# Kernel tuning notes

Measured on AMD Instinct MI355X. Metric: run time of the kernel, lower is better.

The kernel has to match this reference:

```python
import jax, jax.numpy as jnp
import numpy as np

DIM = 1024
HEADS = 16
DIM_HEAD = 64
INNER = HEADS * DIM_HEAD  # 1024
SCALE = DIM_HEAD ** -0.5


def setup_inputs() -> dict:
    key = jax.random.key(0)
    k_x, k_qkv, k_ow, k_ob = jax.random.split(key, 4)
    B, N = 4, 2048
    x = jax.random.normal(k_x, (B, N, DIM), dtype=jnp.float32)
    # nn.Linear weights stored as [out, in] in torch; keep [in, out] for x @ W.
    w_qkv = jax.random.normal(k_qkv, (DIM, 3 * INNER), dtype=jnp.float32) * (DIM ** -0.5)
    w_out = jax.random.normal(k_ow, (INNER, DIM), dtype=jnp.float32) * (INNER ** -0.5)
    b_out = jax.random.normal(k_ob, (DIM,), dtype=jnp.float32) * 0.01
    return {"x": x, "w_qkv": w_qkv, "w_out": w_out, "b_out": b_out}


def reference(x, w_qkv, w_out, b_out):
    B, N, _ = x.shape
    qkv = x @ w_qkv  # [B, N, 3*inner]
    q, k, v = jnp.split(qkv, 3, axis=-1)
    # [B, N, inner] -> [B, H, N, dh]
    def to_heads(t):
        return t.reshape(B, N, HEADS, DIM_HEAD).transpose(0, 2, 1, 3)
    q, k, v = to_heads(q), to_heads(k), to_heads(v)
    attn = jnp.einsum("bhqd,bhkd->bhqk", q, k) * SCALE  # [B, H, N, N]
    attn = jax.nn.softmax(attn, axis=-1)
    out = jnp.einsum("bhqk,bhkd->bhqd", attn, v)  # [B, H, N, dh]
    out = out.transpose(0, 2, 1, 3).reshape(B, N, INNER)
    return out @ w_out + b_out
```

## Files before the change

### kernel.cpp

```cpp
#include <hip/hip_runtime.h>
#include <hip/hip_bf16.h>
#include <stdint.h>

typedef __attribute__((ext_vector_type(4))) float f32x4;
typedef __attribute__((ext_vector_type(8))) short s16x8;
typedef __attribute__((ext_vector_type(4))) short s16x4;

#define DEV static __device__ __forceinline__

constexpr int B_ = 4, H_ = 16, N_ = 2048;
constexpr float CL_ = 0.18033688011112042f;

DEV short f2bf(float x) {
  __hip_bfloat16 h = __float2bfloat16(x);
  return *reinterpret_cast<short*>(&h);
}

DEV uint32_t cvtpk(float lo, float hi) {
  uint32_t r;
  asm("v_cvt_pk_bf16_f32 %0, %1, %2" : "=v"(r) : "v"(lo), "v"(hi));
  return r;
}

DEV void gload16(const void* g, void* l) {
  __builtin_amdgcn_global_load_lds((const __attribute__((address_space(1))) void*)g,
                                   (__attribute__((address_space(3))) void*)l, 16, 0, 0);
}

__global__ void k_cvt(const float* __restrict__ x, short* __restrict__ xb) {
  int i = (blockIdx.x * 256 + threadIdx.x) * 8;
  const float4* p = reinterpret_cast<const float4*>(x + i);
  float4 a = p[0], b = p[1];
  s16x8 o;
  o[0] = f2bf(a.x); o[1] = f2bf(a.y); o[2] = f2bf(a.z); o[3] = f2bf(a.w);
  o[4] = f2bf(b.x); o[5] = f2bf(b.y); o[6] = f2bf(b.z); o[7] = f2bf(b.w);
  *reinterpret_cast<s16x8*>(xb + i) = o;
}

__global__ void k_tw(const float* __restrict__ W, short* __restrict__ WT, int R, int C) {
  __shared__ short t[64][72];
  int r0 = blockIdx.y * 64, c0 = blockIdx.x * 64;
  int tid = threadIdx.x;
  int r = tid >> 2, cp = (tid & 3) * 16;
  const float4* s4 = reinterpret_cast<const float4*>(W + (size_t)(r0 + r) * C + c0 + cp);
  float4 f0 = s4[0], f1 = s4[1], f2 = s4[2], f3 = s4[3];
  short* tr = &t[r][cp];
  tr[0] = f2bf(f0.x); tr[1] = f2bf(f0.y); tr[2]  = f2bf(f0.z); tr[3]  = f2bf(f0.w);
  tr[4] = f2bf(f1.x); tr[5] = f2bf(f1.y); tr[6]  = f2bf(f1.z); tr[7]  = f2bf(f1.w);
  tr[8] = f2bf(f2.x); tr[9] = f2bf(f2.y); tr[10] = f2bf(f2.z); tr[11] = f2bf(f2.w);
  tr[12] = f2bf(f3.x); tr[13] = f2bf(f3.y); tr[14] = f2bf(f3.z); tr[15] = f2bf(f3.w);
  __syncthreads();
  int cc = tid >> 2, rp = (tid & 3) * 16;
  short buf[16];
#pragma unroll
  for (int i = 0; i < 16; ++i) buf[i] = t[rp + i][cc];
  short* dst = WT + (size_t)(c0 + cc) * R + r0 + rp;
  *reinterpret_cast<s16x8*>(dst) = *reinterpret_cast<s16x8*>(buf);
  *reinterpret_cast<s16x8*>(dst + 8) = *reinterpret_cast<s16x8*>(buf + 8);
}

__global__ void k_tv(const short* __restrict__ v, short* __restrict__ vT) {
  __shared__ short t[64][72];
  int bh = blockIdx.y, n0 = blockIdx.x * 64;
  int tid = threadIdx.x;
  int r = tid >> 2, cp = (tid & 3) * 16;
  const short* src = v + ((size_t)bh * N_ + n0 + r) * 64 + cp;
  *reinterpret_cast<s16x8*>(&t[r][cp]) = *reinterpret_cast<const s16x8*>(src);
  *reinterpret_cast<s16x8*>(&t[r][cp + 8]) = *reinterpret_cast<const s16x8*>(src + 8);
  __syncthreads();
  int d = tid >> 2, np = (tid & 3) * 16;
  short buf[16];
#pragma unroll
  for (int i = 0; i < 16; ++i) buf[i] = t[np + i][d];
  short* dst = vT + ((size_t)bh * 64 + d) * N_ + n0 + np;
  *reinterpret_cast<s16x8*>(dst) = *reinterpret_cast<s16x8*>(buf);
  *reinterpret_cast<s16x8*>(dst + 8) = *reinterpret_cast<s16x8*>(buf + 8);
}

template <int EPI>
__global__ __launch_bounds__(256, 2)
void k_gemm(const short* __restrict__ A, const short* __restrict__ BT,
            int M, int N, int K,
            short* __restrict__ oq, short* __restrict__ ok, short* __restrict__ ov,
            const float* __restrict__ bias, float* __restrict__ out) {
  __shared__ short As[128 * 32];
  __shared__ short Bs[128 * 32];
  const int tid = threadIdx.x;
  const int m0 = blockIdx.x * 128, n0 = blockIdx.y * 128;
  const int lane = tid & 63, w = tid >> 6, g = lane >> 4, c = lane & 15;
  const int wr = w >> 1, wc = w & 1;
  f32x4 acc[4][4] = {};
  const int trow = tid >> 2, tk = (tid & 3) * 8;
  const short* ga = A + (size_t)(m0 + trow) * K + tk;
  const short* gb = BT + (size_t)(n0 + trow) * K + tk;
  short* la = As + tid * 8;
  short* lb = Bs + tid * 8;
  for (int k0 = 0; k0 < K; k0 += 32) {
    gload16(ga + k0, la);
    gload16(ga + (size_t)64 * K + k0, la + 2048);
    gload16(gb + k0, lb);
    gload16(gb + (size_t)64 * K + k0, lb + 2048);
    __syncthreads();
    s16x8 af[4], bf[4];
#pragma unroll
    for (int i = 0; i < 4; ++i)
      af[i] = *reinterpret_cast<const s16x8*>(As + (wr * 64 + i * 16 + c) * 32 + g * 8);
#pragma unroll
    for (int j = 0; j < 4; ++j)
      bf[j] = *reinterpret_cast<const s16x8*>(Bs + (wc * 64 + j * 16 + c) * 32 + g * 8);
#pragma unroll
    for (int i = 0; i < 4; ++i)
#pragma unroll
      for (int j = 0; j < 4; ++j)
        acc[i][j] = __builtin_amdgcn_mfma_f32_16x16x32_bf16(af[i], bf[j], acc[i][j], 0, 0, 0);
    __syncthreads();
  }
  if (EPI == 0) {
#pragma unroll
    for (int bj = 0; bj < 4; ++bj) {
      int ncol = n0 + wc * 64 + bj * 16 + c;
      int part = ncol >> 10;
      int c10 = ncol & 1023;
      int h = c10 >> 6, d = c10 & 63;
      short* dst0 = part == 0 ? oq : (part == 1 ? ok : ov);
      float qs = (part == 0) ? CL_ : 1.0f;
#pragma unroll
      for (int ai = 0; ai < 4; ++ai) {
#pragma unroll
        for (int r = 0; r < 4; ++r) {
          int mrow = m0 + wr * 64 + ai * 16 + g * 4 + r;
          int b = mrow >> 11, nr = mrow & 2047;
          dst0[((size_t)((b * H_ + h) * N_ + nr) << 6) + d] = f2bf(acc[ai][bj][r] * qs);
        }
      }
    }
  } else {
#pragma unroll
    for (int bj = 0; bj < 4; ++bj) {
      int ncol = n0 + wc * 64 + bj * 16 + c;
      float bb = bias[ncol];
#pragma unroll
      for (int ai = 0; ai < 4; ++ai) {
#pragma unroll
        for (int r = 0; r < 4; ++r) {
          int mrow = m0 + wr * 64 + ai * 16 + g * 4 + r;
          out[(size_t)mrow * N + ncol] = acc[ai][bj][r] + bb;
        }
      }
    }
  }
}

__global__ __launch_bounds__(512, 4)
void k_attn(const short* __restrict__ q, const short* __restrict__ kk,
            const short* __restrict__ vT, short* __restrict__ ao) {
  __shared__ __align__(16) char smem[65536];
  int qb = blockIdx.x, bh = blockIdx.y;
  int b = bh >> 4, h = bh & 15;
  int tid = threadIdx.x, w = tid >> 6, lane = tid & 63, g = lane >> 4, c = lane & 15;
  char* Pn = smem + 32768 + w * 4096;
  const size_t ho = (size_t)bh * (N_ * 64);
  const char* Kc = reinterpret_cast<const char*>(kk + ho);
  const char* Vc = reinterpret_cast<const char*>(vT + ho);
  const short* Q = q + ho;
  int q0 = qb * 256 + w * 32;
  s16x8 qf[2][2];
#pragma unroll
  for (int i = 0; i < 2; ++i)
#pragma unroll
    for (int ks = 0; ks < 2; ++ks)
      qf[i][ks] = *reinterpret_cast<const s16x8*>(Q + (q0 + i * 16 + c) * 64 + ks * 32 + g * 8);
  f32x4 ot[4][2] = {};
  float lp[2] = {0.f, 0.f};
  const int xsw = (c & 7) << 4;
  const int sr = tid >> 3;
  const int sxo = ((tid & 7) << 4) ^ ((sr & 7) << 4);
  {
    char* base = smem;
    gload16(Kc + (size_t)sr * 128 + sxo, base + tid * 16);
    gload16(Vc + (size_t)sr * 4096 + sxo, base + 8192 + tid * 16);
  }
  __syncthreads();
  int cur = 0;
  for (int tt = 0; tt < N_ / 64; ++tt) {
    if (tt + 1 < N_ / 64) {
      char* base = smem + (cur ^ 1) * 16384;
      gload16(Kc + (size_t)((tt + 1) * 64 + sr) * 128 + sxo, base + tid * 16);
      gload16(Vc + (size_t)sr * 4096 + (tt + 1) * 128 + sxo, base + 8192 + tid * 16);
    }
    const char* kb = smem + cur * 16384;
    const char* vb = kb + 8192;
    s16x8 kf[4][2];
#pragma unroll
    for (int j = 0; j < 4; ++j)
#pragma unroll
      for (int ks = 0; ks < 2; ++ks)
        kf[j][ks] = *reinterpret_cast<const s16x8*>(kb + (j * 16 + c) * 128 + ((ks * 64 + g * 16) ^ xsw));
    f32x4 st[4][2] = {};
    __builtin_amdgcn_s_setprio(1);
#pragma unroll
    for (int j = 0; j < 4; ++j)
#pragma unroll
      for (int i = 0; i < 2; ++i)
#pragma unroll
        for (int ks = 0; ks < 2; ++ks)
          st[j][i] = __builtin_amdgcn_mfma_f32_16x16x32_bf16(kf[j][ks], qf[i][ks], st[j][i], 0, 0, 0);
    __builtin_amdgcn_s_setprio(0);
#pragma unroll
    for (int i = 0; i < 2; ++i) {
#pragma unroll
      for (int j = 0; j < 4; ++j) {
        float p0 = __builtin_amdgcn_exp2f(st[j][i][0]);
        float p1 = __builtin_amdgcn_exp2f(st[j][i][1]);
        float p2 = __builtin_amdgcn_exp2f(st[j][i][2]);
        float p3 = __builtin_amdgcn_exp2f(st[j][i][3]);
        lp[i] += (p0 + p1) + (p2 + p3);
        uint2 pk;
        pk.x = cvtpk(p0, p1);
        pk.y = cvtpk(p2, p3);
        *reinterpret_cast<uint2*>(Pn + i * 2048 + c * 128 + ((j * 32 + g * 8) ^ xsw)) = pk;
      }
    }
    s16x8 pf[2][2];
#pragma unroll
    for (int i = 0; i < 2; ++i)
#pragma unroll
      for (int h2 = 0; h2 < 2; ++h2)
        pf[i][h2] = *reinterpret_cast<const s16x8*>(Pn + i * 2048 + c * 128 + ((h2 * 64 + g * 16) ^ xsw));
    s16x8 vf[4][2];
#pragma unroll
    for (int df = 0; df < 4; ++df)
#pragma unroll
      for (int h2 = 0; h2 < 2; ++h2)
        vf[df][h2] = *reinterpret_cast<const s16x8*>(vb + (df * 16 + c) * 128 + ((h2 * 64 + g * 16) ^ xsw));
    __builtin_amdgcn_s_setprio(1);
#pragma unroll
    for (int df = 0; df < 4; ++df)
#pragma unroll
      for (int i = 0; i < 2; ++i)
#pragma unroll
        for (int h2 = 0; h2 < 2; ++h2)
          ot[df][i] = __builtin_amdgcn_mfma_f32_16x16x32_bf16(vf[df][h2], pf[i][h2], ot[df][i], 0, 0, 0);
    __builtin_amdgcn_s_setprio(0);
    __syncthreads();
    cur ^= 1;
  }
  float ls[2];
#pragma unroll
  for (int i = 0; i < 2; ++i) {
    float t = lp[i];
    t += __shfl_xor(t, 16, 64);
    t += __shfl_xor(t, 32, 64);
    ls[i] = t;
  }
  float inv[2] = {1.f / ls[0], 1.f / ls[1]};
  __syncthreads();
  short* Oq = reinterpret_cast<short*>(smem) + w * 2560;
#pragma unroll
  for (int df = 0; df < 4; ++df)
#pragma unroll
    for (int i = 0; i < 2; ++i) {
      uint2 pk;
      pk.x = cvtpk(ot[df][i][0] * inv[i], ot[df][i][1] * inv[i]);
      pk.y = cvtpk(ot[df][i][2] * inv[i], ot[df][i][3] * inv[i]);
      *reinterpret_cast<uint2*>(Oq + (i * 16 + c) * 80 + df * 16 + g * 4) = pk;
    }
  int q2 = lane >> 1, dp = (lane & 1) * 32;
  size_t ro = (size_t)(b * N_ + q0 + q2) * 1024 + h * 64 + dp;
#pragma unroll
  for (int ch = 0; ch < 4; ++ch) {
    s16x8 vv = *reinterpret_cast<const s16x8*>(Oq + q2 * 80 + dp + ch * 8);
    *reinterpret_cast<s16x8*>(ao + ro + ch * 8) = vv;
  }
}

extern "C" void kernel_launch(void* const* d_in, const int* in_sizes, int n_in,
                              void* d_out, int out_size, void* d_ws, size_t ws_size,
                              hipStream_t stream) {
  const float* x = (const float*)d_in[0];
  const float* w_qkv = (const float*)d_in[1];
  const float* w_out = (const float*)d_in[2];
  const float* b_out = (const float*)d_in[3];
  float* out = (float*)d_out;
  char* ws = (char*)d_ws;
  short* xb    = (short*)(ws);
  short* wqkvT = (short*)(ws + 16777216);
  short* woutT = (short*)(ws + 23068672);
  short* qB    = (short*)(ws + 25165824);
  short* kB    = (short*)(ws + 41943040);
  short* vtmp  = (short*)(ws + 58720256);
  short* vTT   = (short*)(ws + 75497472);
  short* ao    = xb;

  k_cvt<<<4096, 256, 0, stream>>>(x, xb);
  k_tw<<<dim3(48, 16), 256, 0, stream>>>(w_qkv, wqkvT, 1024, 3072);
  k_tw<<<dim3(16, 16), 256, 0, stream>>>(w_out, woutT, 1024, 1024);
  k_gemm<0><<<dim3(64, 24), 256, 0, stream>>>(xb, wqkvT, 8192, 3072, 1024,
                                              qB, kB, vtmp, nullptr, nullptr);
  k_tv<<<dim3(32, 64), 256, 0, stream>>>(vtmp, vTT);
  k_attn<<<dim3(8, 64), 512, 0, stream>>>(qB, kB, vTT, ao);
  k_gemm<1><<<dim3(64, 8), 256, 0, stream>>>(ao, woutT, 8192, 1024, 1024,
                                             nullptr, nullptr, nullptr, b_out, out);
}
```

Baseline: 192.0 us.

## Switch attention to 32x32 MFMA with register-resident P via permlane32 swap

```diff
diff --git a/kernel.cpp b/kernel.cpp
--- a/kernel.cpp
+++ b/kernel.cpp
@@ -3,8 +3,10 @@
 #include <stdint.h>
 
 typedef __attribute__((ext_vector_type(4))) float f32x4;
+typedef __attribute__((ext_vector_type(16))) float f32x16;
 typedef __attribute__((ext_vector_type(8))) short s16x8;
 typedef __attribute__((ext_vector_type(4))) short s16x4;
+typedef __attribute__((ext_vector_type(4))) unsigned int u32x4;
 
 #define DEV static __device__ __forceinline__
 
@@ -151,126 +153,136 @@
   }
 }
 
-__global__ __launch_bounds__(512, 4)
+__global__ __launch_bounds__(256, 2)
 void k_attn(const short* __restrict__ q, const short* __restrict__ kk,
             const short* __restrict__ vT, short* __restrict__ ao) {
-  __shared__ __align__(16) char smem[65536];
-  int qb = blockIdx.x, bh = blockIdx.y;
-  int b = bh >> 4, h = bh & 15;
-  int tid = threadIdx.x, w = tid >> 6, lane = tid & 63, g = lane >> 4, c = lane & 15;
-  char* Pn = smem + 32768 + w * 4096;
+  __shared__ __align__(16) char smem[32768];
+  int bh = blockIdx.x, qb = blockIdx.y;
+  int b = bh >> 4, head = bh & 15;
+  int tid = threadIdx.x, w = tid >> 6, lane = tid & 63;
+  int half = lane >> 5, qc = lane & 31;
   const size_t ho = (size_t)bh * (N_ * 64);
   const char* Kc = reinterpret_cast<const char*>(kk + ho);
   const char* Vc = reinterpret_cast<const char*>(vT + ho);
   const short* Q = q + ho;
-  int q0 = qb * 256 + w * 32;
-  s16x8 qf[2][2];
+  int q0w = qb * 256 + w * 64;
+  s16x8 qf[2][4];
 #pragma unroll
   for (int i = 0; i < 2; ++i)
 #pragma unroll
-    for (int ks = 0; ks < 2; ++ks)
-      qf[i][ks] = *reinterpret_cast<const s16x8*>(Q + (q0 + i * 16 + c) * 64 + ks * 32 + g * 8);
-  f32x4 ot[4][2] = {};
+    for (int ks = 0; ks < 4; ++ks)
+      qf[i][ks] = *reinterpret_cast<const s16x8*>(Q + (size_t)(q0w + i * 32 + qc) * 64 + ks * 16 + half * 8);
+  f32x16 ot[2][2] = {};
   float lp[2] = {0.f, 0.f};
-  const int xsw = (c & 7) << 4;
-  const int sr = tid >> 3;
-  const int sxo = ((tid & 7) << 4) ^ ((sr & 7) << 4);
+  const int rsw = (qc & 7) << 4;
+  const int s_i0 = tid, s_i1 = tid + 256;
+  const int s_r0 = s_i0 >> 3, s_c0 = ((s_i0 & 7) << 4) ^ ((s_r0 & 7) << 4);
+  const int s_r1 = s_i1 >> 3, s_c1 = ((s_i1 & 7) << 4) ^ ((s_r1 & 7) << 4);
   {
-    char* base = smem;
-    gload16(Kc + (size_t)sr * 128 + sxo, base + tid * 16);
-    gload16(Vc + (size_t)sr * 4096 + sxo, base + 8192 + tid * 16);
+    char* kb_ = smem;
+    gload16(Kc + (size_t)s_r0 * 128 + s_c0, kb_ + s_i0 * 16);
+    gload16(Kc + (size_t)s_r1 * 128 + s_c1, kb_ + s_i1 * 16);
+    gload16(Vc + (size_t)s_r0 * 4096 + s_c0, kb_ + 8192 + s_i0 * 16);
+    gload16(Vc + (size_t)s_r1 * 4096 + s_c1, kb_ + 8192 + s_i1 * 16);
   }
   __syncthreads();
   int cur = 0;
   for (int tt = 0; tt < N_ / 64; ++tt) {
     if (tt + 1 < N_ / 64) {
-      char* base = smem + (cur ^ 1) * 16384;
-      gload16(Kc + (size_t)((tt + 1) * 64 + sr) * 128 + sxo, base + tid * 16);
-      gload16(Vc + (size_t)sr * 4096 + (tt + 1) * 128 + sxo, base + 8192 + tid * 16);
+      char* nb = smem + (cur ^ 1) * 16384;
+      gload16(Kc + (size_t)((tt + 1) * 64 + s_r0) * 128 + s_c0, nb + s_i0 * 16);
+      gload16(Kc + (size_t)((tt + 1) * 64 + s_r1) * 128 + s_c1, nb + s_i1 * 16);
+      gload16(Vc + (size_t)s_r0 * 4096 + (tt + 1) * 128 + s_c0, nb + 8192 + s_i0 * 16);
+      gload16(Vc + (size_t)s_r1 * 4096 + (tt + 1) * 128 + s_c1, nb + 8192 + s_i1 * 16);
     }
-    const char* kb = smem + cur * 16384;
-    const char* vb = kb + 8192;
-    s16x8 kf[4][2];
-#pragma unroll
-    for (int j = 0; j < 4; ++j)
-#pragma unroll
-      for (int ks = 0; ks < 2; ++ks)
-        kf[j][ks] = *reinterpret_cast<const s16x8*>(kb + (j * 16 + c) * 128 + ((ks * 64 + g * 16) ^ xsw));
-    f32x4 st[4][2] = {};
+    const char* kb_ = smem + cur * 16384;
+    const char* vb_ = kb_ + 8192;
+    s16x8 kf[2][4];
+#pragma unroll
+    for (int j = 0; j < 2; ++j)
+#pragma unroll
+      for (int ks = 0; ks < 4; ++ks)
+        kf[j][ks] = *reinterpret_cast<const s16x8*>(kb_ + (j * 32 + qc) * 128 + ((ks * 32 + half * 16) ^ rsw));
+    f32x16 st[2][2] = {};
     __builtin_amdgcn_s_setprio(1);
 #pragma unroll
-    for (int j = 0; j < 4; ++j)
+    for (int j = 0; j < 2; ++j)
 #pragma unroll
       for (int i = 0; i < 2; ++i)
 #pragma unroll
-        for (int ks = 0; ks < 2; ++ks)
-          st[j][i] = __builtin_amdgcn_mfma_f32_16x16x32_bf16(kf[j][ks], qf[i][ks], st[j][i], 0, 0, 0);
+        for (int ks = 0; ks < 4; ++ks)
+          st[j][i] = __builtin_amdgcn_mfma_f32_32x32x16_bf16(kf[j][ks], qf[i][ks], st[j][i], 0, 0, 0);
     __builtin_amdgcn_s_setprio(0);
 #pragma unroll
-    for (int i = 0; i < 2; ++i) {
-#pragma unroll
-      for (int j = 0; j < 4; ++j) {
-        float p0 = __builtin_amdgcn_exp2f(st[j][i][0]);
-        float p1 = __builtin_amdgcn_exp2f(st[j][i][1]);
-        float p2 = __builtin_amdgcn_exp2f(st[j][i][2]);
-        float p3 = __builtin_amdgcn_exp2f(st[j][i][3]);
-        lp[i] += (p0 + p1) + (p2 + p3);
-        uint2 pk;
-        pk.x = cvtpk(p0, p1);
-        pk.y = cvtpk(p2, p3);
-        *reinterpret_cast<uint2*>(Pn + i * 2048 + c * 128 + ((j * 32 + g * 8) ^ xsw)) = pk;
-      }
-    }
-    s16x8 pf[2][2];
-#pragma unroll
-    for (int i = 0; i < 2; ++i)
-#pragma unroll
-      for (int h2 = 0; h2 < 2; ++h2)
-        pf[i][h2] = *reinterpret_cast<const s16x8*>(Pn + i * 2048 + c * 128 + ((h2 * 64 + g * 16) ^ xsw));
-    s16x8 vf[4][2];
-#pragma unroll
-    for (int df = 0; df < 4; ++df)
-#pragma unroll
-      for (int h2 = 0; h2 < 2; ++h2)
-        vf[df][h2] = *reinterpret_cast<const s16x8*>(vb + (df * 16 + c) * 128 + ((h2 * 64 + g * 16) ^ xsw));
+    for (int j = 0; j < 2; ++j)
+#pragma unroll
+      for (int i = 0; i < 2; ++i)
+#pragma unroll
+        for (int r = 0; r < 16; ++r) {
+          float p = __builtin_amdgcn_exp2f(st[j][i][r]);
+          st[j][i][r] = p;
+          lp[i] += p;
+        }
+    u32x4 pwv[2][4];
+#pragma unroll
+    for (int j = 0; j < 2; ++j)
+#pragma unroll
+      for (int i = 0; i < 2; ++i)
+#pragma unroll
+        for (int bb = 0; bb < 2; ++bb)
+#pragma unroll
+          for (int p = 0; p < 2; ++p) {
+            uint32_t Aw = cvtpk(st[j][i][8 * bb + 2 * p], st[j][i][8 * bb + 2 * p + 1]);
+            uint32_t Bw = cvtpk(st[j][i][8 * bb + 4 + 2 * p], st[j][i][8 * bb + 4 + 2 * p + 1]);
+            asm volatile("v_permlane32_swap_b32 %0, %1" : "+v"(Aw), "+v"(Bw));
+            pwv[i][j * 2 + bb][p] = Aw;
+            pwv[i][j * 2 + bb][p + 2] = Bw;
+          }
+    s16x8 vf[2][4];
+#pragma unroll
+    for (int db = 0; db < 2; ++db)
+#pragma unroll
+      for (int kb4 = 0; kb4 < 4; ++kb4)
+        vf[db][kb4] = *reinterpret_cast<const s16x8*>(vb_ + (db * 32 + qc) * 128 + ((kb4 * 32 + half * 16) ^ rsw));
     __builtin_amdgcn_s_setprio(1);
 #pragma unroll
-    for (int df = 0; df < 4; ++df)
+    for (int db = 0; db < 2; ++db)
 #pragma unroll
       for (int i = 0; i < 2; ++i)
 #pragma unroll
-        for (int h2 = 0; h2 < 2; ++h2)
-          ot[df][i] = __builtin_amdgcn_mfma_f32_16x16x32_bf16(vf[df][h2], pf[i][h2], ot[df][i], 0, 0, 0);
+        for (int kb4 = 0; kb4 < 4; ++kb4)
+          ot[db][i] = __builtin_amdgcn_mfma_f32_32x32x16_bf16(
+              vf[db][kb4], __builtin_bit_cast(s16x8, pwv[i][kb4]), ot[db][i], 0, 0, 0);
     __builtin_amdgcn_s_setprio(0);
     __syncthreads();
     cur ^= 1;
   }
-  float ls[2];
+  float inv[2];
 #pragma unroll
   for (int i = 0; i < 2; ++i) {
-    float t = lp[i];
-    t += __shfl_xor(t, 16, 64);
-    t += __shfl_xor(t, 32, 64);
-    ls[i] = t;
-  }
-  float inv[2] = {1.f / ls[0], 1.f / ls[1]};
+    float t = lp[i] + __shfl_xor(lp[i], 32, 64);
+    inv[i] = 1.f / t;
+  }
   __syncthreads();
-  short* Oq = reinterpret_cast<short*>(smem) + w * 2560;
-#pragma unroll
-  for (int df = 0; df < 4; ++df)
-#pragma unroll
-    for (int i = 0; i < 2; ++i) {
-      uint2 pk;
-      pk.x = cvtpk(ot[df][i][0] * inv[i], ot[df][i][1] * inv[i]);
-      pk.y = cvtpk(ot[df][i][2] * inv[i], ot[df][i][3] * inv[i]);
-      *reinterpret_cast<uint2*>(Oq + (i * 16 + c) * 80 + df * 16 + g * 4) = pk;
+  short* Oq = reinterpret_cast<short*>(smem) + w * 2304;
+#pragma unroll
+  for (int i = 0; i < 2; ++i) {
+#pragma unroll
+    for (int db = 0; db < 2; ++db)
+#pragma unroll
+      for (int m = 0; m < 4; ++m) {
+        uint2 pk;
+        pk.x = cvtpk(ot[db][i][4 * m] * inv[i], ot[db][i][4 * m + 1] * inv[i]);
+        pk.y = cvtpk(ot[db][i][4 * m + 2] * inv[i], ot[db][i][4 * m + 3] * inv[i]);
+        *reinterpret_cast<uint2*>(Oq + qc * 72 + db * 32 + m * 8 + half * 4) = pk;
+      }
+    int q2 = lane >> 1, dcol = (lane & 1) * 32;
+    size_t ro = (size_t)(b * N_ + q0w + i * 32 + q2) * 1024 + head * 64 + dcol;
+#pragma unroll
+    for (int ch = 0; ch < 4; ++ch) {
+      s16x8 vv = *reinterpret_cast<const s16x8*>(Oq + q2 * 72 + dcol + ch * 8);
+      *reinterpret_cast<s16x8*>(ao + ro + ch * 8) = vv;
     }
-  int q2 = lane >> 1, dp = (lane & 1) * 32;
-  size_t ro = (size_t)(b * N_ + q0 + q2) * 1024 + h * 64 + dp;
-#pragma unroll
-  for (int ch = 0; ch < 4; ++ch) {
-    s16x8 vv = *reinterpret_cast<const s16x8*>(Oq + q2 * 80 + dp + ch * 8);
-    *reinterpret_cast<s16x8*>(ao + ro + ch * 8) = vv;
   }
 }
 
@@ -298,7 +310,7 @@
   k_gemm<0><<<dim3(64, 24), 256, 0, stream>>>(xb, wqkvT, 8192, 3072, 1024,
                                               qB, kB, vtmp, nullptr, nullptr);
   k_tv<<<dim3(32, 64), 256, 0, stream>>>(vtmp, vTT);
-  k_attn<<<dim3(8, 64), 512, 0, stream>>>(qB, kB, vTT, ao);
+  k_attn<<<dim3(64, 8), 256, 0, stream>>>(qB, kB, vTT, ao);
   k_gemm<1><<<dim3(64, 8), 256, 0, stream>>>(ao, woutT, 8192, 1024, 1024,
                                              nullptr, nullptr, nullptr, b_out, out);
 }
```

New measurement: 193.8 us. About the same (+0.9%).
